# Performance work log

Hardware: AMD Instinct MI355X
Metric: run time of the kernel (lower is better)

The kernel has to match this reference:

```python
import jax, jax.numpy as jnp
import numpy as np

EPS = 1e-12  # torch F.normalize eps

def _normalize(x):
    n = jnp.sqrt(jnp.sum(x * x, axis=-1, keepdims=True))
    return x / jnp.maximum(n, EPS)

def bgs_extended(d6s):
    # d6s: [B, N, D, 3, 2] -> rotation [B, N, D, 3, 3] (columns b1,b2,b3)
    b1 = _normalize(d6s[..., :, 0])
    a2 = d6s[..., :, 1]
    dot = jnp.sum(b1 * a2, axis=-1, keepdims=True)
    b2 = _normalize(a2 - dot * b1)
    b3 = jnp.cross(b1, b2, axis=-1)
    return jnp.stack([b1, b2, b3], axis=-1)

def setup_inputs() -> dict:
    key = jax.random.key(0)
    k1, k2, k3, k4, k5 = jax.random.split(key, 5)
    B, N, D, F = 8, 8192, 64, 64
    X = jax.random.normal(k1, (B, N, D, 3), dtype=jnp.float32)
    J = jax.random.normal(k2, (B, N, D, 3, 2), dtype=jnp.float32)
    A = jax.random.normal(k3, (F, D), dtype=jnp.float32)
    Bm = jax.random.normal(k4, (F, D), dtype=jnp.float32)
    C = jax.random.normal(k5, (F, D), dtype=jnp.float32)
    return {"X": X, "J": J, "A": A, "Bm": Bm, "C": C}

def reference(X, J, A, Bm, C):
    R = bgs_extended(J)  # [B,N,D,3,3]
    # RT_i X = dot(column i of R, X) -> compute all three at once: [B,N,D,3]
    RTX = jnp.einsum('bndki,bndk->bndi', R, X)
    rt0, rt1, rt2 = RTX[..., 0:1], RTX[..., 1:2], RTX[..., 2:3]
    # get_rrtx(i, R, s) == R[..., :, i] * s
    a_term = R[..., :, 0] * rt0 + R[..., :, 1] * rt1
    b_term = R[..., :, 1] * rt0 - R[..., :, 0] * rt1
    c_term = R[..., :, 2] * rt2
    Y = (jnp.einsum('fe,bnei->bnfi', A, a_term)
         + jnp.einsum('fe,bnei->bnfi', Bm, b_term)
         + jnp.einsum('fe,bnei->bnfi', C, c_term))
    return Y
```

## Files before the change

### kernel.cpp

```cpp
#include <hip/hip_runtime.h>

typedef __bf16 bf16;
typedef bf16 bf16x8 __attribute__((ext_vector_type(8)));
typedef float f32x4 __attribute__((ext_vector_type(4)));

#define PTS 16
#define NG 4
#define WREG 4800

__device__ __forceinline__ void load_group(
    const float* __restrict__ J, const float* __restrict__ X,
    long bn0, int wave, int lane, float jv[4][6], float xv[4][3])
{
    const float* jg = J + (bn0 + wave * 4) * 384 + lane * 6;
    #pragma unroll
    for (int q = 0; q < 4; ++q) {
        float2 ja = *(const float2*)(jg + q * 384 + 0);
        float2 jb = *(const float2*)(jg + q * 384 + 2);
        float2 jc2 = *(const float2*)(jg + q * 384 + 4);
        jv[q][0] = ja.x; jv[q][1] = ja.y;
        jv[q][2] = jb.x; jv[q][3] = jb.y;
        jv[q][4] = jc2.x; jv[q][5] = jc2.y;
    }
    const float* xg = X + (bn0 + wave * 4) * 192 + lane * 3;
    #pragma unroll
    for (int q = 0; q < 4; ++q) {
        xv[q][0] = xg[q * 192 + 0];
        xv[q][1] = xg[q * 192 + 1];
        xv[q][2] = xg[q * 192 + 2];
    }
}

__global__ __launch_bounds__(256, 4)
void affine_linear_fused(const float* __restrict__ X, const float* __restrict__ J,
                         const float* __restrict__ A, const float* __restrict__ Bm,
                         const float* __restrict__ C, float* __restrict__ Y)
{
    __shared__ __attribute__((aligned(128))) unsigned char lds[4 * WREG];

    const int tid  = threadIdx.x;
    const int wave = tid >> 6;
    const int lane = tid & 63;
    const int l16  = lane & 15;
    const int lq   = lane >> 4;
    unsigned char* wbase = &lds[wave * WREG];

    const long gbase = (long)blockIdx.x * NG;

    float jc[4][6], xc[4][3];
    load_group(J, X, gbase * PTS, wave, lane, jc, xc);

    const int f = wave * 16 + l16;
    bf16x8 wfrag[6];
    #pragma unroll
    for (int kk = 0; kk < 6; ++kk) {
        const float* src = (kk < 2) ? A : (kk < 4) ? Bm : C;
        const f32x4* p4 = (const f32x4*)(src + f * 64 + (kk & 1) * 32 + lq * 8);
        f32x4 lo = p4[0], hi = p4[1];
        bf16x8 w;
        w[0] = (bf16)lo[0]; w[1] = (bf16)lo[1]; w[2] = (bf16)lo[2]; w[3] = (bf16)lo[3];
        w[4] = (bf16)hi[0]; w[5] = (bf16)hi[1]; w[6] = (bf16)hi[2]; w[7] = (bf16)hi[3];
        wfrag[kk] = w;
    }

    const unsigned char* arow[3];
    #pragma unroll
    for (int mt = 0; mt < 3; ++mt) {
        int m  = mt * 16 + l16;
        int wv = m / 12;
        int r  = m - wv * 12;
        arow[mt] = &lds[wv * WREG + r * 400] + lq * 16;
    }

    #pragma unroll
    for (int g = 0; g < NG; ++g) {
        float jn[4][6], xn[4][3];
        if (g + 1 < NG)
            load_group(J, X, (gbase + g + 1) * PTS, wave, lane, jn, xn);

        const long bn0 = (gbase + g) * PTS;

        #pragma unroll
        for (int q = 0; q < 4; ++q) {
            float a1x = jc[q][0], a2x = jc[q][1];
            float a1y = jc[q][2], a2y = jc[q][3];
            float a1z = jc[q][4], a2z = jc[q][5];
            float xx = xc[q][0], xy = xc[q][1], xz = xc[q][2];

            float n1sq = a1x*a1x + a1y*a1y + a1z*a1z;
            float inv1 = __builtin_amdgcn_rsqf(fmaxf(n1sq, 1e-24f));
            float b1x = a1x*inv1, b1y = a1y*inv1, b1z = a1z*inv1;
            float dot = b1x*a2x + b1y*a2y + b1z*a2z;
            float ux = a2x - dot*b1x, uy = a2y - dot*b1y, uz = a2z - dot*b1z;
            float n2sq = ux*ux + uy*uy + uz*uz;
            float inv2 = __builtin_amdgcn_rsqf(fmaxf(n2sq, 1e-24f));
            float b2x = ux*inv2, b2y = uy*inv2, b2z = uz*inv2;
            float b3x = b1y*b2z - b1z*b2y;
            float b3y = b1z*b2x - b1x*b2z;
            float b3z = b1x*b2y - b1y*b2x;

            float rt0 = b1x*xx + b1y*xy + b1z*xz;
            float rt1 = b2x*xx + b2y*xy + b2z*xz;
            float rt2 = b3x*xx + b3y*xy + b3z*xz;

            float at0 = b1x*rt0 + b2x*rt1;
            float at1 = b1y*rt0 + b2y*rt1;
            float at2 = b1z*rt0 + b2z*rt1;
            float bt0 = b2x*rt0 - b1x*rt1;
            float bt1 = b2y*rt0 - b1y*rt1;
            float bt2 = b2z*rt0 - b1z*rt1;
            float ct0 = b3x*rt2, ct1 = b3y*rt2, ct2 = b3z*rt2;

            bf16* r0 = (bf16*)(wbase + (q*3 + 0) * 400);
            bf16* r1 = (bf16*)(wbase + (q*3 + 1) * 400);
            bf16* r2 = (bf16*)(wbase + (q*3 + 2) * 400);
            r0[lane] = (bf16)at0; r0[64+lane] = (bf16)bt0; r0[128+lane] = (bf16)ct0;
            r1[lane] = (bf16)at1; r1[64+lane] = (bf16)bt1; r1[128+lane] = (bf16)ct1;
            r2[lane] = (bf16)at2; r2[64+lane] = (bf16)bt2; r2[128+lane] = (bf16)ct2;
        }

        __asm__ volatile("s_waitcnt lgkmcnt(0)" ::: "memory");
        __builtin_amdgcn_s_barrier();

        f32x4 acc[3];
        #pragma unroll
        for (int mt = 0; mt < 3; ++mt) acc[mt] = (f32x4){0.f, 0.f, 0.f, 0.f};
        #pragma unroll
        for (int kk = 0; kk < 6; ++kk) {
            #pragma unroll
            for (int mt = 0; mt < 3; ++mt) {
                bf16x8 af = *(const bf16x8*)(arow[mt] + kk * 64);
                acc[mt] = __builtin_amdgcn_mfma_f32_16x16x32_bf16(af, wfrag[kk], acc[mt], 0, 0, 0);
            }
        }

        __asm__ volatile("s_waitcnt lgkmcnt(0)" ::: "memory");
        __builtin_amdgcn_s_barrier();

        float* yw = (float*)wbase;
        #pragma unroll
        for (int mt = 0; mt < 3; ++mt) {
            #pragma unroll
            for (int r = 0; r < 4; ++r) {
                int m  = mt * 16 + lq * 4 + r;
                int wv = m / 12;
                int rr = m - wv * 12;
                int q  = rr / 3;
                int i  = rr - q * 3;
                int p  = wv * 4 + q;
                yw[p * 48 + l16 * 3 + i] = acc[mt][r];
            }
        }

        const f32x4* ysrc = (const f32x4*)yw;
        #pragma unroll
        for (int v = 0; v < 3; ++v) {
            int vi = v * 64 + lane;
            int p  = vi / 12;
            int vo = vi - p * 12;
            f32x4* dst = (f32x4*)(Y + (bn0 + p) * 192 + wave * 48) + vo;
            *dst = ysrc[vi];
        }

        if (g + 1 < NG) {
            #pragma unroll
            for (int q = 0; q < 4; ++q) {
                #pragma unroll
                for (int k = 0; k < 6; ++k) jc[q][k] = jn[q][k];
                #pragma unroll
                for (int k = 0; k < 3; ++k) xc[q][k] = xn[q][k];
            }
        }
    }
}

extern "C" void kernel_launch(void* const* d_in, const int* in_sizes, int n_in,
                              void* d_out, int out_size, void* d_ws, size_t ws_size,
                              hipStream_t stream) {
    const float* X  = (const float*)d_in[0];
    const float* J  = (const float*)d_in[1];
    const float* A  = (const float*)d_in[2];
    const float* Bm = (const float*)d_in[3];
    const float* C  = (const float*)d_in[4];
    float* Y = (float*)d_out;

    const int points = in_sizes[0] / (64 * 3);
    const int blocks = points / (PTS * NG);
    affine_linear_fused<<<blocks, 256, 0, stream>>>(X, J, A, Bm, C, Y);
}
```

Measured before the change: 206.7 us.

## Make each wave own its 16 points and all 64 outputs, removing block barriers

Each wave now processes 16 consecutive points end to end and computes all 64 output features for its own 48 rows, so no data is shared between waves. This removes the two block barriers per group that existed when waves cooperated on a shared A tile. The trade-offs are a fourfold larger per-wave LDS region (about 77KB per block), which is why launch bounds drop to 2 blocks per CU. Weight fragments are now reloaded from global memory and converted to bf16 per n-tile, and each wave holds 12 accumulator tiles instead of 3, raising register pressure.

```diff
diff --git a/kernel.cpp b/kernel.cpp
--- a/kernel.cpp
+++ b/kernel.cpp
@@ -4,25 +4,22 @@
 typedef bf16 bf16x8 __attribute__((ext_vector_type(8)));
 typedef float f32x4 __attribute__((ext_vector_type(4)));
 
-#define PTS 16
-#define NG 4
-#define WREG 4800
+#define WREG 19200
 
-__device__ __forceinline__ void load_group(
-    const float* __restrict__ J, const float* __restrict__ X,
-    long bn0, int wave, int lane, float jv[4][6], float xv[4][3])
+__device__ __forceinline__ void load4(const float* __restrict__ J, const float* __restrict__ X,
+                                      long p0, int lane, float jv[4][6], float xv[4][3])
 {
-    const float* jg = J + (bn0 + wave * 4) * 384 + lane * 6;
+    const float* jg = J + p0 * 384 + lane * 6;
     #pragma unroll
     for (int q = 0; q < 4; ++q) {
-        float2 ja = *(const float2*)(jg + q * 384 + 0);
-        float2 jb = *(const float2*)(jg + q * 384 + 2);
+        float2 ja  = *(const float2*)(jg + q * 384 + 0);
+        float2 jb  = *(const float2*)(jg + q * 384 + 2);
         float2 jc2 = *(const float2*)(jg + q * 384 + 4);
-        jv[q][0] = ja.x; jv[q][1] = ja.y;
-        jv[q][2] = jb.x; jv[q][3] = jb.y;
+        jv[q][0] = ja.x;  jv[q][1] = ja.y;
+        jv[q][2] = jb.x;  jv[q][3] = jb.y;
         jv[q][4] = jc2.x; jv[q][5] = jc2.y;
     }
-    const float* xg = X + (bn0 + wave * 4) * 192 + lane * 3;
+    const float* xg = X + p0 * 192 + lane * 3;
     #pragma unroll
     for (int q = 0; q < 4; ++q) {
         xv[q][0] = xg[q * 192 + 0];
@@ -31,7 +28,7 @@
     }
 }
 
-__global__ __launch_bounds__(256, 4)
+__global__ __launch_bounds__(256, 2)
 void affine_linear_fused(const float* __restrict__ X, const float* __restrict__ J,
                          const float* __restrict__ A, const float* __restrict__ Bm,
                          const float* __restrict__ C, float* __restrict__ Y)
@@ -44,41 +41,15 @@
     const int l16  = lane & 15;
     const int lq   = lane >> 4;
     unsigned char* wbase = &lds[wave * WREG];
-
-    const long gbase = (long)blockIdx.x * NG;
+    const long bn0 = (long)blockIdx.x * 64 + wave * 16;
 
     float jc[4][6], xc[4][3];
-    load_group(J, X, gbase * PTS, wave, lane, jc, xc);
-
-    const int f = wave * 16 + l16;
-    bf16x8 wfrag[6];
-    #pragma unroll
-    for (int kk = 0; kk < 6; ++kk) {
-        const float* src = (kk < 2) ? A : (kk < 4) ? Bm : C;
-        const f32x4* p4 = (const f32x4*)(src + f * 64 + (kk & 1) * 32 + lq * 8);
-        f32x4 lo = p4[0], hi = p4[1];
-        bf16x8 w;
-        w[0] = (bf16)lo[0]; w[1] = (bf16)lo[1]; w[2] = (bf16)lo[2]; w[3] = (bf16)lo[3];
-        w[4] = (bf16)hi[0]; w[5] = (bf16)hi[1]; w[6] = (bf16)hi[2]; w[7] = (bf16)hi[3];
-        wfrag[kk] = w;
-    }
-
-    const unsigned char* arow[3];
-    #pragma unroll
-    for (int mt = 0; mt < 3; ++mt) {
-        int m  = mt * 16 + l16;
-        int wv = m / 12;
-        int r  = m - wv * 12;
-        arow[mt] = &lds[wv * WREG + r * 400] + lq * 16;
-    }
+    load4(J, X, bn0, lane, jc, xc);
 
     #pragma unroll
-    for (int g = 0; g < NG; ++g) {
+    for (int s = 0; s < 4; ++s) {
         float jn[4][6], xn[4][3];
-        if (g + 1 < NG)
-            load_group(J, X, (gbase + g + 1) * PTS, wave, lane, jn, xn);
-
-        const long bn0 = (gbase + g) * PTS;
+        if (s < 3) load4(J, X, bn0 + (s + 1) * 4, lane, jn, xn);
 
         #pragma unroll
         for (int q = 0; q < 4; ++q) {
@@ -111,58 +82,16 @@
             float bt2 = b2z*rt0 - b1z*rt1;
             float ct0 = b3x*rt2, ct1 = b3y*rt2, ct2 = b3z*rt2;
 
-            bf16* r0 = (bf16*)(wbase + (q*3 + 0) * 400);
-            bf16* r1 = (bf16*)(wbase + (q*3 + 1) * 400);
-            bf16* r2 = (bf16*)(wbase + (q*3 + 2) * 400);
+            const int row = (s * 4 + q) * 3;
+            bf16* r0 = (bf16*)(wbase + (row + 0) * 400);
+            bf16* r1 = (bf16*)(wbase + (row + 1) * 400);
+            bf16* r2 = (bf16*)(wbase + (row + 2) * 400);
             r0[lane] = (bf16)at0; r0[64+lane] = (bf16)bt0; r0[128+lane] = (bf16)ct0;
             r1[lane] = (bf16)at1; r1[64+lane] = (bf16)bt1; r1[128+lane] = (bf16)ct1;
             r2[lane] = (bf16)at2; r2[64+lane] = (bf16)bt2; r2[128+lane] = (bf16)ct2;
         }
 
-        __asm__ volatile("s_waitcnt lgkmcnt(0)" ::: "memory");
-        __builtin_amdgcn_s_barrier();
-
-        f32x4 acc[3];
-        #pragma unroll
-        for (int mt = 0; mt < 3; ++mt) acc[mt] = (f32x4){0.f, 0.f, 0.f, 0.f};
-        #pragma unroll
-        for (int kk = 0; kk < 6; ++kk) {
-            #pragma unroll
-            for (int mt = 0; mt < 3; ++mt) {
-                bf16x8 af = *(const bf16x8*)(arow[mt] + kk * 64);
-                acc[mt] = __builtin_amdgcn_mfma_f32_16x16x32_bf16(af, wfrag[kk], acc[mt], 0, 0, 0);
-            }
-        }
-
-        __asm__ volatile("s_waitcnt lgkmcnt(0)" ::: "memory");
-        __builtin_amdgcn_s_barrier();
-
-        float* yw = (float*)wbase;
-        #pragma unroll
-        for (int mt = 0; mt < 3; ++mt) {
-            #pragma unroll
-            for (int r = 0; r < 4; ++r) {
-                int m  = mt * 16 + lq * 4 + r;
-                int wv = m / 12;
-                int rr = m - wv * 12;
-                int q  = rr / 3;
-                int i  = rr - q * 3;
-                int p  = wv * 4 + q;
-                yw[p * 48 + l16 * 3 + i] = acc[mt][r];
-            }
-        }
-
-        const f32x4* ysrc = (const f32x4*)yw;
-        #pragma unroll
-        for (int v = 0; v < 3; ++v) {
-            int vi = v * 64 + lane;
-            int p  = vi / 12;
-            int vo = vi - p * 12;
-            f32x4* dst = (f32x4*)(Y + (bn0 + p) * 192 + wave * 48) + vo;
-            *dst = ysrc[vi];
-        }
-
-        if (g + 1 < NG) {
+        if (s < 3) {
             #pragma unroll
             for (int q = 0; q < 4; ++q) {
                 #pragma unroll
@@ -172,6 +101,69 @@
             }
         }
     }
+
+    __asm__ volatile("s_waitcnt lgkmcnt(0)" ::: "memory");
+
+    const unsigned char* arow[3];
+    #pragma unroll
+    for (int mt = 0; mt < 3; ++mt)
+        arow[mt] = wbase + (mt * 16 + l16) * 400 + lq * 16;
+
+    f32x4 acc[3][4];
+    #pragma unroll
+    for (int mt = 0; mt < 3; ++mt)
+        #pragma unroll
+        for (int nt = 0; nt < 4; ++nt)
+            acc[mt][nt] = (f32x4){0.f, 0.f, 0.f, 0.f};
+
+    #pragma unroll
+    for (int nt = 0; nt < 4; ++nt) {
+        const int f = nt * 16 + l16;
+        f32x4 wlo[6], whi[6];
+        #pragma unroll
+        for (int kk = 0; kk < 6; ++kk) {
+            const float* src = (kk < 2) ? A : (kk < 4) ? Bm : C;
+            const f32x4* p4 = (const f32x4*)(src + f * 64 + (kk & 1) * 32 + lq * 8);
+            wlo[kk] = p4[0];
+            whi[kk] = p4[1];
+        }
+        #pragma unroll
+        for (int kk = 0; kk < 6; ++kk) {
+            bf16x8 w;
+            w[0] = (bf16)wlo[kk][0]; w[1] = (bf16)wlo[kk][1];
+            w[2] = (bf16)wlo[kk][2]; w[3] = (bf16)wlo[kk][3];
+            w[4] = (bf16)whi[kk][0]; w[5] = (bf16)whi[kk][1];
+            w[6] = (bf16)whi[kk][2]; w[7] = (bf16)whi[kk][3];
+            #pragma unroll
+            for (int mt = 0; mt < 3; ++mt) {
+                bf16x8 af = *(const bf16x8*)(arow[mt] + kk * 64);
+                acc[mt][nt] = __builtin_amdgcn_mfma_f32_16x16x32_bf16(af, w, acc[mt][nt], 0, 0, 0);
+            }
+        }
+    }
+
+    __asm__ volatile("s_waitcnt lgkmcnt(0)" ::: "memory");
+
+    float* yw = (float*)wbase;
+    #pragma unroll
+    for (int mt = 0; mt < 3; ++mt)
+        #pragma unroll
+        for (int nt = 0; nt < 4; ++nt)
+            #pragma unroll
+            for (int r = 0; r < 4; ++r) {
+                int m = mt * 16 + lq * 4 + r;
+                int p = m / 3;
+                int i = m - p * 3;
+                yw[p * 192 + (nt * 16 + l16) * 3 + i] = acc[mt][nt][r];
+            }
+
+    __asm__ volatile("s_waitcnt lgkmcnt(0)" ::: "memory");
+
+    const f32x4* ysrc = (const f32x4*)yw;
+    f32x4* ydst = (f32x4*)(Y + bn0 * 192);
+    #pragma unroll
+    for (int v = 0; v < 12; ++v)
+        ydst[v * 64 + lane] = ysrc[v * 64 + lane];
 }
 
 extern "C" void kernel_launch(void* const* d_in, const int* in_sizes, int n_in,
@@ -185,6 +177,6 @@
     float* Y = (float*)d_out;
 
     const int points = in_sizes[0] / (64 * 3);
-    const int blocks = points / (PTS * NG);
+    const int blocks = points / 64;
     affine_linear_fused<<<blocks, 256, 0, stream>>>(X, J, A, Bm, C, Y);
 }
```

After: 218.3 us. 1.06x slower.

## Load J directly into LDS and process one point group per block

Applied to the files above, without the earlier changes.

Drops the per-block loop over four point groups and its register prefetch, launching four times as many blocks that each handle one 16-point group. J is now fetched with 16-byte coalesced global_load_lds transfers straight into each wave's LDS region, which is enlarged to hold it, and then read back per lane for the Gram-Schmidt math. The launch-bounds occupancy hint rises from 4 to 6. The intent is better coalescing of the 6-float J records and more latency hiding through occupancy. In exchange it loses the software prefetch overlap and reloads and converts the weight fragments in every block.

```diff
diff --git a/kernel.cpp b/kernel.cpp
--- a/kernel.cpp
+++ b/kernel.cpp
@@ -3,35 +3,18 @@
 typedef __bf16 bf16;
 typedef bf16 bf16x8 __attribute__((ext_vector_type(8)));
 typedef float f32x4 __attribute__((ext_vector_type(4)));
+typedef unsigned int u32;
 
 #define PTS 16
-#define NG 4
-#define WREG 4800
+#define WREG 6144
 
-__device__ __forceinline__ void load_group(
-    const float* __restrict__ J, const float* __restrict__ X,
-    long bn0, int wave, int lane, float jv[4][6], float xv[4][3])
-{
-    const float* jg = J + (bn0 + wave * 4) * 384 + lane * 6;
-    #pragma unroll
-    for (int q = 0; q < 4; ++q) {
-        float2 ja = *(const float2*)(jg + q * 384 + 0);
-        float2 jb = *(const float2*)(jg + q * 384 + 2);
-        float2 jc2 = *(const float2*)(jg + q * 384 + 4);
-        jv[q][0] = ja.x; jv[q][1] = ja.y;
-        jv[q][2] = jb.x; jv[q][3] = jb.y;
-        jv[q][4] = jc2.x; jv[q][5] = jc2.y;
-    }
-    const float* xg = X + (bn0 + wave * 4) * 192 + lane * 3;
-    #pragma unroll
-    for (int q = 0; q < 4; ++q) {
-        xv[q][0] = xg[q * 192 + 0];
-        xv[q][1] = xg[q * 192 + 1];
-        xv[q][2] = xg[q * 192 + 2];
-    }
+__device__ __forceinline__ void gld_lds16(const void* g, void* l) {
+    __builtin_amdgcn_global_load_lds(
+        (const __attribute__((address_space(1))) u32*)g,
+        (__attribute__((address_space(3))) u32*)l, 16, 0, 0);
 }
 
-__global__ __launch_bounds__(256, 4)
+__global__ __launch_bounds__(256, 6)
 void affine_linear_fused(const float* __restrict__ X, const float* __restrict__ J,
                          const float* __restrict__ A, const float* __restrict__ Bm,
                          const float* __restrict__ C, float* __restrict__ Y)
@@ -43,25 +26,97 @@
     const int lane = tid & 63;
     const int l16  = lane & 15;
     const int lq   = lane >> 4;
+    const long bn0 = (long)blockIdx.x * PTS;
+
     unsigned char* wbase = &lds[wave * WREG];
 
-    const long gbase = (long)blockIdx.x * NG;
+    {
+        const float* jg = J + (bn0 + wave * 4) * 384;
+        #pragma unroll
+        for (int t = 0; t < 6; ++t)
+            gld_lds16(jg + t * 256 + lane * 4, wbase + t * 1024);
+    }
 
-    float jc[4][6], xc[4][3];
-    load_group(J, X, gbase * PTS, wave, lane, jc, xc);
+    float xv[4][3];
+    {
+        const float* xg = X + (bn0 + wave * 4) * 192 + lane * 3;
+        #pragma unroll
+        for (int q = 0; q < 4; ++q) {
+            xv[q][0] = xg[q * 192 + 0];
+            xv[q][1] = xg[q * 192 + 1];
+            xv[q][2] = xg[q * 192 + 2];
+        }
+    }
 
     const int f = wave * 16 + l16;
-    bf16x8 wfrag[6];
+    f32x4 wlo[6], whi[6];
     #pragma unroll
     for (int kk = 0; kk < 6; ++kk) {
         const float* src = (kk < 2) ? A : (kk < 4) ? Bm : C;
         const f32x4* p4 = (const f32x4*)(src + f * 64 + (kk & 1) * 32 + lq * 8);
-        f32x4 lo = p4[0], hi = p4[1];
+        wlo[kk] = p4[0];
+        whi[kk] = p4[1];
+    }
+
+    __asm__ volatile("s_waitcnt vmcnt(0)" ::: "memory");
+
+    bf16x8 wfrag[6];
+    #pragma unroll
+    for (int kk = 0; kk < 6; ++kk) {
         bf16x8 w;
-        w[0] = (bf16)lo[0]; w[1] = (bf16)lo[1]; w[2] = (bf16)lo[2]; w[3] = (bf16)lo[3];
-        w[4] = (bf16)hi[0]; w[5] = (bf16)hi[1]; w[6] = (bf16)hi[2]; w[7] = (bf16)hi[3];
+        w[0] = (bf16)wlo[kk][0]; w[1] = (bf16)wlo[kk][1];
+        w[2] = (bf16)wlo[kk][2]; w[3] = (bf16)wlo[kk][3];
+        w[4] = (bf16)whi[kk][0]; w[5] = (bf16)whi[kk][1];
+        w[6] = (bf16)whi[kk][2]; w[7] = (bf16)whi[kk][3];
         wfrag[kk] = w;
     }
+
+    const float* jlds = (const float*)wbase;
+    #pragma unroll
+    for (int q = 0; q < 4; ++q) {
+        const float* jp = jlds + q * 384 + lane * 6;
+        float2 ja  = *(const float2*)(jp + 0);
+        float2 jb  = *(const float2*)(jp + 2);
+        float2 jc2 = *(const float2*)(jp + 4);
+        float a1x = ja.x,  a2x = ja.y;
+        float a1y = jb.x,  a2y = jb.y;
+        float a1z = jc2.x, a2z = jc2.y;
+        float xx = xv[q][0], xy = xv[q][1], xz = xv[q][2];
+
+        float n1sq = a1x*a1x + a1y*a1y + a1z*a1z;
+        float inv1 = __builtin_amdgcn_rsqf(fmaxf(n1sq, 1e-24f));
+        float b1x = a1x*inv1, b1y = a1y*inv1, b1z = a1z*inv1;
+        float dot = b1x*a2x + b1y*a2y + b1z*a2z;
+        float ux = a2x - dot*b1x, uy = a2y - dot*b1y, uz = a2z - dot*b1z;
+        float n2sq = ux*ux + uy*uy + uz*uz;
+        float inv2 = __builtin_amdgcn_rsqf(fmaxf(n2sq, 1e-24f));
+        float b2x = ux*inv2, b2y = uy*inv2, b2z = uz*inv2;
+        float b3x = b1y*b2z - b1z*b2y;
+        float b3y = b1z*b2x - b1x*b2z;
+        float b3z = b1x*b2y - b1y*b2x;
+
+        float rt0 = b1x*xx + b1y*xy + b1z*xz;
+        float rt1 = b2x*xx + b2y*xy + b2z*xz;
+        float rt2 = b3x*xx + b3y*xy + b3z*xz;
+
+        float at0 = b1x*rt0 + b2x*rt1;
+        float at1 = b1y*rt0 + b2y*rt1;
+        float at2 = b1z*rt0 + b2z*rt1;
+        float bt0 = b2x*rt0 - b1x*rt1;
+        float bt1 = b2y*rt0 - b1y*rt1;
+        float bt2 = b2z*rt0 - b1z*rt1;
+        float ct0 = b3x*rt2, ct1 = b3y*rt2, ct2 = b3z*rt2;
+
+        bf16* r0 = (bf16*)(wbase + (q*3 + 0) * 400);
+        bf16* r1 = (bf16*)(wbase + (q*3 + 1) * 400);
+        bf16* r2 = (bf16*)(wbase + (q*3 + 2) * 400);
+        r0[lane] = (bf16)at0; r0[64+lane] = (bf16)bt0; r0[128+lane] = (bf16)ct0;
+        r1[lane] = (bf16)at1; r1[64+lane] = (bf16)bt1; r1[128+lane] = (bf16)ct1;
+        r2[lane] = (bf16)at2; r2[64+lane] = (bf16)bt2; r2[128+lane] = (bf16)ct2;
+    }
+
+    __asm__ volatile("s_waitcnt lgkmcnt(0)" ::: "memory");
+    __builtin_amdgcn_s_barrier();
 
     const unsigned char* arow[3];
     #pragma unroll
@@ -71,106 +126,44 @@
         int r  = m - wv * 12;
         arow[mt] = &lds[wv * WREG + r * 400] + lq * 16;
     }
-
+    f32x4 acc[3];
     #pragma unroll
-    for (int g = 0; g < NG; ++g) {
-        float jn[4][6], xn[4][3];
-        if (g + 1 < NG)
-            load_group(J, X, (gbase + g + 1) * PTS, wave, lane, jn, xn);
-
-        const long bn0 = (gbase + g) * PTS;
-
-        #pragma unroll
-        for (int q = 0; q < 4; ++q) {
-            float a1x = jc[q][0], a2x = jc[q][1];
-            float a1y = jc[q][2], a2y = jc[q][3];
-            float a1z = jc[q][4], a2z = jc[q][5];
-            float xx = xc[q][0], xy = xc[q][1], xz = xc[q][2];
-
-            float n1sq = a1x*a1x + a1y*a1y + a1z*a1z;
-            float inv1 = __builtin_amdgcn_rsqf(fmaxf(n1sq, 1e-24f));
-            float b1x = a1x*inv1, b1y = a1y*inv1, b1z = a1z*inv1;
-            float dot = b1x*a2x + b1y*a2y + b1z*a2z;
-            float ux = a2x - dot*b1x, uy = a2y - dot*b1y, uz = a2z - dot*b1z;
-            float n2sq = ux*ux + uy*uy + uz*uz;
-            float inv2 = __builtin_amdgcn_rsqf(fmaxf(n2sq, 1e-24f));
-            float b2x = ux*inv2, b2y = uy*inv2, b2z = uz*inv2;
-            float b3x = b1y*b2z - b1z*b2y;
-            float b3y = b1z*b2x - b1x*b2z;
-            float b3z = b1x*b2y - b1y*b2x;
-
-            float rt0 = b1x*xx + b1y*xy + b1z*xz;
-            float rt1 = b2x*xx + b2y*xy + b2z*xz;
-            float rt2 = b3x*xx + b3y*xy + b3z*xz;
-
-            float at0 = b1x*rt0 + b2x*rt1;
-            float at1 = b1y*rt0 + b2y*rt1;
-            float at2 = b1z*rt0 + b2z*rt1;
-            float bt0 = b2x*rt0 - b1x*rt1;
-            float bt1 = b2y*rt0 - b1y*rt1;
-            float bt2 = b2z*rt0 - b1z*rt1;
-            float ct0 = b3x*rt2, ct1 = b3y*rt2, ct2 = b3z*rt2;
-
-            bf16* r0 = (bf16*)(wbase + (q*3 + 0) * 400);
-            bf16* r1 = (bf16*)(wbase + (q*3 + 1) * 400);
-            bf16* r2 = (bf16*)(wbase + (q*3 + 2) * 400);
-            r0[lane] = (bf16)at0; r0[64+lane] = (bf16)bt0; r0[128+lane] = (bf16)ct0;
-            r1[lane] = (bf16)at1; r1[64+lane] = (bf16)bt1; r1[128+lane] = (bf16)ct1;
-            r2[lane] = (bf16)at2; r2[64+lane] = (bf16)bt2; r2[128+lane] = (bf16)ct2;
-        }
-
-        __asm__ volatile("s_waitcnt lgkmcnt(0)" ::: "memory");
-        __builtin_amdgcn_s_barrier();
-
-        f32x4 acc[3];
-        #pragma unroll
-        for (int mt = 0; mt < 3; ++mt) acc[mt] = (f32x4){0.f, 0.f, 0.f, 0.f};
-        #pragma unroll
-        for (int kk = 0; kk < 6; ++kk) {
-            #pragma unroll
-            for (int mt = 0; mt < 3; ++mt) {
-                bf16x8 af = *(const bf16x8*)(arow[mt] + kk * 64);
-                acc[mt] = __builtin_amdgcn_mfma_f32_16x16x32_bf16(af, wfrag[kk], acc[mt], 0, 0, 0);
-            }
-        }
-
-        __asm__ volatile("s_waitcnt lgkmcnt(0)" ::: "memory");
-        __builtin_amdgcn_s_barrier();
-
-        float* yw = (float*)wbase;
+    for (int mt = 0; mt < 3; ++mt) acc[mt] = (f32x4){0.f, 0.f, 0.f, 0.f};
+    #pragma unroll
+    for (int kk = 0; kk < 6; ++kk) {
         #pragma unroll
         for (int mt = 0; mt < 3; ++mt) {
-            #pragma unroll
-            for (int r = 0; r < 4; ++r) {
-                int m  = mt * 16 + lq * 4 + r;
-                int wv = m / 12;
-                int rr = m - wv * 12;
-                int q  = rr / 3;
-                int i  = rr - q * 3;
-                int p  = wv * 4 + q;
-                yw[p * 48 + l16 * 3 + i] = acc[mt][r];
-            }
+            bf16x8 af = *(const bf16x8*)(arow[mt] + kk * 64);
+            acc[mt] = __builtin_amdgcn_mfma_f32_16x16x32_bf16(af, wfrag[kk], acc[mt], 0, 0, 0);
         }
+    }
 
-        const f32x4* ysrc = (const f32x4*)yw;
+    __asm__ volatile("s_waitcnt lgkmcnt(0)" ::: "memory");
+    __builtin_amdgcn_s_barrier();
+
+    float* yw = (float*)wbase;
+    #pragma unroll
+    for (int mt = 0; mt < 3; ++mt) {
         #pragma unroll
-        for (int v = 0; v < 3; ++v) {
-            int vi = v * 64 + lane;
-            int p  = vi / 12;
-            int vo = vi - p * 12;
-            f32x4* dst = (f32x4*)(Y + (bn0 + p) * 192 + wave * 48) + vo;
-            *dst = ysrc[vi];
+        for (int r = 0; r < 4; ++r) {
+            int m  = mt * 16 + lq * 4 + r;
+            int wv = m / 12;
+            int rr = m - wv * 12;
+            int q  = rr / 3;
+            int i  = rr - q * 3;
+            int p  = wv * 4 + q;
+            yw[p * 48 + l16 * 3 + i] = acc[mt][r];
         }
+    }
 
-        if (g + 1 < NG) {
-            #pragma unroll
-            for (int q = 0; q < 4; ++q) {
-                #pragma unroll
-                for (int k = 0; k < 6; ++k) jc[q][k] = jn[q][k];
-                #pragma unroll
-                for (int k = 0; k < 3; ++k) xc[q][k] = xn[q][k];
-            }
-        }
+    const f32x4* ysrc = (const f32x4*)yw;
+    #pragma unroll
+    for (int v = 0; v < 3; ++v) {
+        int vi = v * 64 + lane;
+        int p  = vi / 12;
+        int vo = vi - p * 12;
+        f32x4* dst = (f32x4*)(Y + (bn0 + p) * 192 + wave * 48) + vo;
+        *dst = ysrc[vi];
     }
 }
 
@@ -185,6 +178,6 @@
     float* Y = (float*)d_out;
 
     const int points = in_sizes[0] / (64 * 3);
-    const int blocks = points / (PTS * NG);
+    const int blocks = points / PTS;
     affine_linear_fused<<<blocks, 256, 0, stream>>>(X, J, A, Bm, C, Y);
 }
```

After: 205.8 us. No clear change (-0.5%).
